# Kernel tuning notes

Hardware: AMD Instinct MI355X
Metric: run time of the kernel (lower is better)

The kernel has to match this reference:

```python
import jax, jax.numpy as jnp
import numpy as np

GAMMA = 0.96875      # retention decay, 1 - 2**-5
GROUPS = 8           # config.group_norm_num
EPS = 1e-6           # config.retention_group_norm_eps


def _get_D(T, dtype):
    # D[n, m] = gamma**(n-m) for n >= m else 0 (causal exponential decay)
    n = jnp.arange(T)[:, None]
    m = jnp.arange(T)[None, :]
    log_g = jnp.log(jnp.asarray(GAMMA, dtype))
    # where-select avoids inf*0 NaNs for n < m (matches D[D != D] = 0)
    return jnp.where(n >= m, jnp.exp((n - m).astype(dtype) * log_g),
                     jnp.zeros((), dtype))


def _group_norm(x, w, b):
    # x: (N, C); torch.nn.GroupNorm semantics (biased variance, affine)
    N, C = x.shape
    xg = x.reshape(N, GROUPS, C // GROUPS)
    mu = xg.mean(-1, keepdims=True)
    var = xg.var(-1, keepdims=True)
    xn = ((xg - mu) * jax.lax.rsqrt(var + EPS)).reshape(N, C)
    return xn * w + b


def setup_inputs() -> dict:
    key = jax.random.key(0)
    k0, k1, k2, k3, k4 = jax.random.split(key, 5)
    B, T, C = 2, 8192, 64
    Q_in = jax.random.normal(k0, (B, T, C), jnp.float32)
    W_Q = jax.random.normal(k1, (C, C), jnp.float32) / C
    W_K = jax.random.normal(k2, (C, C), jnp.float32) / C
    W_V = jax.random.normal(k3, (C, C), jnp.float32) / C
    gn_weight = 1.0 + 0.02 * jax.random.normal(k4, (C,), jnp.float32)
    gn_bias = jnp.zeros((C,), jnp.float32)
    return {"Q_in": Q_in, "W_Q": W_Q, "W_K": W_K, "W_V": W_V,
            "gn_weight": gn_weight, "gn_bias": gn_bias}


def reference(Q_in, W_Q, W_K, W_V, gn_weight, gn_bias):
    B, T, C = Q_in.shape
    # _qkv with KV_in=None, act='none'
    Q = Q_in @ W_Q
    K = Q_in @ W_K
    V = Q_in @ W_V
    # retention scores with multiplicative causal decay mask
    QK = jnp.einsum("btc,bsc->bts", Q, K) * _get_D(T, Q.dtype)[None]
    out = jnp.einsum("bts,bsc->btc", QK, V)  # (B, T, C)
    # _out: dropout(p=0) -> GroupNorm over flattened (B*T, C) -> transpose+view
    out = _group_norm(out.reshape(-1, C), gn_weight, gn_bias).reshape(B, T, C)
    out = jnp.swapaxes(out, -2, -1).reshape(B, T, C)  # faithful to .transpose().view()
    return out
```

## Files before the change

### kernel.cpp

```cpp
#include <hip/hip_runtime.h>


constexpr int SEQ = 8192;
constexpr int CH  = 64;
constexpr float LOG2G = -0.045803690f;

typedef __attribute__((ext_vector_type(8))) _Float16     half8;
typedef __attribute__((ext_vector_type(4))) float        f32x4;
typedef __attribute__((ext_vector_type(4))) unsigned int u32x4;

__device__ inline unsigned short f2h(float x) {
    _Float16 h = (_Float16)x;
    return __builtin_bit_cast(unsigned short, h);
}

__global__ __launch_bounds__(256) void qkv_kernel(
    const float* __restrict__ Xin, const float* __restrict__ Wq,
    const float* __restrict__ Wk, const float* __restrict__ Wv,
    unsigned short* __restrict__ Qh, unsigned short* __restrict__ Kh,
    unsigned short* __restrict__ Vt)
{
    __shared__ unsigned short sWt[3][64][72];
    const int tid = threadIdx.x;
    const size_t row0 = (size_t)blockIdx.x * 64;
    const int b  = (int)(row0 >> 13);
    const int t0 = (int)(row0 & (SEQ - 1));

    {
        const int c  = tid & 63;
        const int k0 = (tid >> 6) * 2;
        #pragma unroll
        for (int m = 0; m < 3; ++m) {
            const float* W = (m == 0) ? Wq : ((m == 1) ? Wk : Wv);
            #pragma unroll
            for (int it = 0; it < 8; ++it) {
                const int k = k0 + it * 8;
                const unsigned lo = f2h(W[k * 64 + c]);
                const unsigned hi = f2h(W[(k + 1) * 64 + c]);
                *(unsigned int*)&sWt[m][c][k] = lo | (hi << 16);
            }
        }
    }

    const int l15 = tid & 15, q4 = (tid >> 4) & 3, wvi = tid >> 6;

    half8 xf[2];
    {
        const float* Xp = Xin + (row0 + (size_t)(wvi * 16 + l15)) * 64;
        #pragma unroll
        for (int h = 0; h < 2; ++h) {
            const f32x4 a  = *(const f32x4*)(Xp + h * 32 + q4 * 8);
            const f32x4 bb = *(const f32x4*)(Xp + h * 32 + q4 * 8 + 4);
            half8 t;
            t[0] = (_Float16)a[0];  t[1] = (_Float16)a[1];
            t[2] = (_Float16)a[2];  t[3] = (_Float16)a[3];
            t[4] = (_Float16)bb[0]; t[5] = (_Float16)bb[1];
            t[6] = (_Float16)bb[2]; t[7] = (_Float16)bb[3];
            xf[h] = t;
        }
    }
    __syncthreads();

    const int trow = (int)row0 + wvi * 16;
    #pragma unroll
    for (int m = 0; m < 2; ++m) {
        unsigned short* O = (m == 0) ? Qh : Kh;
        #pragma unroll
        for (int ct = 0; ct < 4; ++ct) {
            const half8 wf0 = *(const half8*)&sWt[m][ct * 16 + l15][q4 * 8];
            const half8 wf1 = *(const half8*)&sWt[m][ct * 16 + l15][32 + q4 * 8];
            f32x4 d = {0.f, 0.f, 0.f, 0.f};
            d = __builtin_amdgcn_mfma_f32_16x16x32_f16(xf[0], wf0, d, 0, 0, 0);
            d = __builtin_amdgcn_mfma_f32_16x16x32_f16(xf[1], wf1, d, 0, 0, 0);
            #pragma unroll
            for (int i = 0; i < 4; ++i)
                O[(size_t)(trow + q4 * 4 + i) * 64 + ct * 16 + l15] = f2h(d[i]);
        }
    }
    #pragma unroll
    for (int mt = 0; mt < 4; ++mt) {
        const half8 wf0 = *(const half8*)&sWt[2][mt * 16 + l15][q4 * 8];
        const half8 wf1 = *(const half8*)&sWt[2][mt * 16 + l15][32 + q4 * 8];
        f32x4 d = {0.f, 0.f, 0.f, 0.f};
        d = __builtin_amdgcn_mfma_f32_16x16x32_f16(wf0, xf[0], d, 0, 0, 0);
        d = __builtin_amdgcn_mfma_f32_16x16x32_f16(wf1, xf[1], d, 0, 0, 0);
        #pragma unroll
        for (int i = 0; i < 4; ++i)
            Vt[(size_t)(b * 64 + mt * 16 + q4 * 4 + i) * SEQ + t0 + wvi * 16 + l15] = f2h(d[i]);
    }
}

__global__ __launch_bounds__(256, 4) void attn_kernel(
    const unsigned short* __restrict__ Qh, const unsigned short* __restrict__ Kh,
    const unsigned short* __restrict__ Vt,
    const float* __restrict__ gnw, const float* __restrict__ gnb,
    float* __restrict__ out)
{
    __shared__ unsigned int sS[4][16][44];
    __shared__ float sO[4][16][68];
    __shared__ float sGW[64], sGB[64];

    const int tid  = threadIdx.x;
    const int w    = tid >> 6;
    const int lane = tid & 63;
    const int l15  = lane & 15, q4 = lane >> 4;
    const int tile = blockIdx.x;
    const int b    = tile >> 9;
    const int t0   = (tile & 511) << 4;

    if (tid < 64) { sGW[tid] = gnw[tid]; sGB[tid] = gnb[tid]; }

    const unsigned short* Qp = Qh + (size_t)(b * SEQ + t0 + l15) * 64 + q4 * 8;
    const half8 qf0 = *(const half8*)Qp;
    const half8 qf1 = *(const half8*)(Qp + 32);

    float g0[4];
    #pragma unroll
    for (int i = 0; i < 4; ++i)
        g0[i] = exp2f((float)(l15 - q4 * 4 - i) * LOG2G);
    const float c16 = exp2f(-16.f * LOG2G);
    const float c32 = c16 * c16;
    const float c48 = c32 * c16;

    f32x4 acc[4];
    #pragma unroll
    for (int ct = 0; ct < 4; ++ct) acc[ct] = (f32x4){0.f, 0.f, 0.f, 0.f};

    const int cs_hi = t0 >> 6;
    const int cs_lo = (cs_hi >= 16) ? cs_hi - 16 : 0;
    const unsigned short* Kbase = Kh + (size_t)b * SEQ * 64;
    const unsigned short* Vbase = Vt + (size_t)b * 64 * SEQ;

    for (int cs = cs_lo + w; cs <= cs_hi; cs += 4) {
        const int s0 = cs << 6;

        half8 kf[4][2];
        #pragma unroll
        for (int st = 0; st < 4; ++st) {
            const unsigned short* p = Kbase + (size_t)(s0 + st * 16 + l15) * 64 + q4 * 8;
            kf[st][0] = *(const half8*)p;
            kf[st][1] = *(const half8*)(p + 32);
        }
        f32x4 sv[4];
        #pragma unroll
        for (int st = 0; st < 4; ++st) {
            f32x4 s = {0.f, 0.f, 0.f, 0.f};
            s = __builtin_amdgcn_mfma_f32_16x16x32_f16(kf[st][0], qf0, s, 0, 0, 0);
            s = __builtin_amdgcn_mfma_f32_16x16x32_f16(kf[st][1], qf1, s, 0, 0, 0);
            sv[st] = s;
        }

        half8 vf[4][2];
        #pragma unroll
        for (int ct = 0; ct < 4; ++ct) {
            const unsigned short* p = Vbase + (size_t)(ct * 16 + l15) * SEQ + s0 + q4 * 8;
            vf[ct][0] = *(const half8*)p;
            vf[ct][1] = *(const half8*)(p + 32);
        }

        const float gbase = exp2f((float)(t0 - s0) * LOG2G);
        const float gs[4] = {gbase, gbase * c16, gbase * c32, gbase * c48};
        if (cs < cs_hi) {
            #pragma unroll
            for (int st = 0; st < 4; ++st) {
                const unsigned u0 = (unsigned)f2h(sv[st][0] * (gs[st] * g0[0]))
                                  | ((unsigned)f2h(sv[st][1] * (gs[st] * g0[1])) << 16);
                const unsigned u1 = (unsigned)f2h(sv[st][2] * (gs[st] * g0[2]))
                                  | ((unsigned)f2h(sv[st][3] * (gs[st] * g0[3])) << 16);
                sS[w][l15][st * 8 + q4 * 2]     = u0;
                sS[w][l15][st * 8 + q4 * 2 + 1] = u1;
            }
        } else {
            const int dbase = t0 + l15 - s0;
            #pragma unroll
            for (int st = 0; st < 4; ++st) {
                float wt[4];
                #pragma unroll
                for (int i = 0; i < 4; ++i) {
                    const int srel = st * 16 + q4 * 4 + i;
                    wt[i] = (dbase - srel >= 0) ? gs[st] * g0[i] : 0.f;
                }
                const unsigned u0 = (unsigned)f2h(sv[st][0] * wt[0])
                                  | ((unsigned)f2h(sv[st][1] * wt[1]) << 16);
                const unsigned u1 = (unsigned)f2h(sv[st][2] * wt[2])
                                  | ((unsigned)f2h(sv[st][3] * wt[3]) << 16);
                sS[w][l15][st * 8 + q4 * 2]     = u0;
                sS[w][l15][st * 8 + q4 * 2 + 1] = u1;
            }
        }

        asm volatile("s_waitcnt lgkmcnt(0)" ::: "memory");

        const u32x4 ua0 = *(const u32x4*)&sS[w][l15][q4 * 4];
        const u32x4 ua1 = *(const u32x4*)&sS[w][l15][16 + q4 * 4];
        const half8 af0 = __builtin_bit_cast(half8, ua0);
        const half8 af1 = __builtin_bit_cast(half8, ua1);
        #pragma unroll
        for (int ct = 0; ct < 4; ++ct) {
            acc[ct] = __builtin_amdgcn_mfma_f32_16x16x32_f16(af0, vf[ct][0], acc[ct], 0, 0, 0);
            acc[ct] = __builtin_amdgcn_mfma_f32_16x16x32_f16(af1, vf[ct][1], acc[ct], 0, 0, 0);
        }
    }

    #pragma unroll
    for (int ct = 0; ct < 4; ++ct) {
        #pragma unroll
        for (int i = 0; i < 4; ++i)
            sO[w][q4 * 4 + i][ct * 16 + l15] = acc[ct][i];
    }
    __syncthreads();
    {
        const int r = tid >> 4, c4 = (tid & 15) * 4;
        f32x4 v = *(const f32x4*)&sO[0][r][c4];
        v += *(const f32x4*)&sO[1][r][c4];
        v += *(const f32x4*)&sO[2][r][c4];
        v += *(const f32x4*)&sO[3][r][c4];
        *(f32x4*)&sO[0][r][c4] = v;
    }
    __syncthreads();
    if (tid < 128) {
        const int r = tid >> 3, g = tid & 7;
        float x[8];
        float s = 0.f, ss = 0.f;
        #pragma unroll
        for (int j = 0; j < 8; ++j) {
            x[j] = sO[0][r][g * 8 + j];
            s += x[j]; ss += x[j] * x[j];
        }
        const float mu  = s * 0.125f;
        const float var = ss * 0.125f - mu * mu;
        const float rs  = rsqrtf(var + 1e-6f);
        #pragma unroll
        for (int j = 0; j < 8; ++j) {
            const int c = g * 8 + j;
            sO[0][r][c] = (x[j] - mu) * rs * sGW[c] + sGB[c];
        }
    }
    __syncthreads();
    #pragma unroll
    for (int pass = 0; pass < 4; ++pass) {
        const int c = pass * 16 + (tid >> 4);
        const int t = tid & 15;
        out[(size_t)(b * 64 + c) * SEQ + t0 + t] = sO[0][t][c];
    }
}

extern "C" void kernel_launch(void* const* d_in, const int* in_sizes, int n_in,
                              void* d_out, int out_size, void* d_ws, size_t ws_size,
                              hipStream_t stream)
{
    const float* Xin = (const float*)d_in[0];
    const float* Wq  = (const float*)d_in[1];
    const float* Wk  = (const float*)d_in[2];
    const float* Wv  = (const float*)d_in[3];
    const float* gnw = (const float*)d_in[4];
    const float* gnb = (const float*)d_in[5];

    const size_t NROW = (size_t)2 * SEQ;
    unsigned short* Qh = (unsigned short*)d_ws;
    unsigned short* Kh = Qh + NROW * CH;
    unsigned short* Vt = Kh + NROW * CH;

    qkv_kernel<<<dim3(256), dim3(256), 0, stream>>>(Xin, Wq, Wk, Wv, Qh, Kh, Vt);
    attn_kernel<<<dim3(1024), dim3(256), 0, stream>>>(Qh, Kh, Vt, gnw, gnb, (float*)d_out);
}
```

Before: 102.8 us.

## Split QKV projection across per-matrix waves with register-held weights

Restructures the QKV projection kernel so each block handles 16 rows with three waves, one each for Q, K and V. Each wave loads and converts its weight matrix straight into registers, which removes the shared-memory staging and the block barrier. The grid grows from 256 to 1024 blocks for more parallelism. In exchange, weight loads from global memory are repeated per block and are strided (uncoalesced), though they should mostly hit in cache.

```diff
diff --git a/kernel.cpp b/kernel.cpp
--- a/kernel.cpp
+++ b/kernel.cpp
@@ -14,79 +14,73 @@
     return __builtin_bit_cast(unsigned short, h);
 }
 
-__global__ __launch_bounds__(256) void qkv_kernel(
+__global__ __launch_bounds__(192) void qkv_kernel(
     const float* __restrict__ Xin, const float* __restrict__ Wq,
     const float* __restrict__ Wk, const float* __restrict__ Wv,
     unsigned short* __restrict__ Qh, unsigned short* __restrict__ Kh,
     unsigned short* __restrict__ Vt)
 {
-    __shared__ unsigned short sWt[3][64][72];
-    const int tid = threadIdx.x;
-    const size_t row0 = (size_t)blockIdx.x * 64;
+    const int tid  = threadIdx.x;
+    const int role = tid >> 6;
+    const int lane = tid & 63;
+    const int l15  = lane & 15, q4 = lane >> 4;
+    const size_t row0 = (size_t)blockIdx.x * 16;
     const int b  = (int)(row0 >> 13);
     const int t0 = (int)(row0 & (SEQ - 1));
 
-    {
-        const int c  = tid & 63;
-        const int k0 = (tid >> 6) * 2;
-        #pragma unroll
-        for (int m = 0; m < 3; ++m) {
-            const float* W = (m == 0) ? Wq : ((m == 1) ? Wk : Wv);
-            #pragma unroll
-            for (int it = 0; it < 8; ++it) {
-                const int k = k0 + it * 8;
-                const unsigned lo = f2h(W[k * 64 + c]);
-                const unsigned hi = f2h(W[(k + 1) * 64 + c]);
-                *(unsigned int*)&sWt[m][c][k] = lo | (hi << 16);
-            }
-        }
-    }
-
-    const int l15 = tid & 15, q4 = (tid >> 4) & 3, wvi = tid >> 6;
-
     half8 xf[2];
     {
-        const float* Xp = Xin + (row0 + (size_t)(wvi * 16 + l15)) * 64;
+        const float* Xp = Xin + (row0 + l15) * 64;
         #pragma unroll
         for (int h = 0; h < 2; ++h) {
-            const f32x4 a  = *(const f32x4*)(Xp + h * 32 + q4 * 8);
-            const f32x4 bb = *(const f32x4*)(Xp + h * 32 + q4 * 8 + 4);
+            const f32x4 a = *(const f32x4*)(Xp + h * 32 + q4 * 8);
+            const f32x4 c = *(const f32x4*)(Xp + h * 32 + q4 * 8 + 4);
             half8 t;
-            t[0] = (_Float16)a[0];  t[1] = (_Float16)a[1];
-            t[2] = (_Float16)a[2];  t[3] = (_Float16)a[3];
-            t[4] = (_Float16)bb[0]; t[5] = (_Float16)bb[1];
-            t[6] = (_Float16)bb[2]; t[7] = (_Float16)bb[3];
+            t[0] = (_Float16)a[0]; t[1] = (_Float16)a[1];
+            t[2] = (_Float16)a[2]; t[3] = (_Float16)a[3];
+            t[4] = (_Float16)c[0]; t[5] = (_Float16)c[1];
+            t[6] = (_Float16)c[2]; t[7] = (_Float16)c[3];
             xf[h] = t;
         }
     }
-    __syncthreads();
-
-    const int trow = (int)row0 + wvi * 16;
-    #pragma unroll
-    for (int m = 0; m < 2; ++m) {
-        unsigned short* O = (m == 0) ? Qh : Kh;
+
+    const float* W = (role == 0) ? Wq : ((role == 1) ? Wk : Wv);
+    half8 wf[4][2];
+    #pragma unroll
+    for (int ct = 0; ct < 4; ++ct) {
+        const int c = ct * 16 + l15;
+        #pragma unroll
+        for (int kh = 0; kh < 2; ++kh) {
+            const int k0 = kh * 32 + q4 * 8;
+            half8 t;
+            #pragma unroll
+            for (int j = 0; j < 8; ++j)
+                t[j] = (_Float16)W[(k0 + j) * 64 + c];
+            wf[ct][kh] = t;
+        }
+    }
+
+    if (role < 2) {
+        unsigned short* O = (role == 0) ? Qh : Kh;
         #pragma unroll
         for (int ct = 0; ct < 4; ++ct) {
-            const half8 wf0 = *(const half8*)&sWt[m][ct * 16 + l15][q4 * 8];
-            const half8 wf1 = *(const half8*)&sWt[m][ct * 16 + l15][32 + q4 * 8];
             f32x4 d = {0.f, 0.f, 0.f, 0.f};
-            d = __builtin_amdgcn_mfma_f32_16x16x32_f16(xf[0], wf0, d, 0, 0, 0);
-            d = __builtin_amdgcn_mfma_f32_16x16x32_f16(xf[1], wf1, d, 0, 0, 0);
+            d = __builtin_amdgcn_mfma_f32_16x16x32_f16(xf[0], wf[ct][0], d, 0, 0, 0);
+            d = __builtin_amdgcn_mfma_f32_16x16x32_f16(xf[1], wf[ct][1], d, 0, 0, 0);
             #pragma unroll
             for (int i = 0; i < 4; ++i)
-                O[(size_t)(trow + q4 * 4 + i) * 64 + ct * 16 + l15] = f2h(d[i]);
-        }
-    }
-    #pragma unroll
-    for (int mt = 0; mt < 4; ++mt) {
-        const half8 wf0 = *(const half8*)&sWt[2][mt * 16 + l15][q4 * 8];
-        const half8 wf1 = *(const half8*)&sWt[2][mt * 16 + l15][32 + q4 * 8];
-        f32x4 d = {0.f, 0.f, 0.f, 0.f};
-        d = __builtin_amdgcn_mfma_f32_16x16x32_f16(wf0, xf[0], d, 0, 0, 0);
-        d = __builtin_amdgcn_mfma_f32_16x16x32_f16(wf1, xf[1], d, 0, 0, 0);
-        #pragma unroll
-        for (int i = 0; i < 4; ++i)
-            Vt[(size_t)(b * 64 + mt * 16 + q4 * 4 + i) * SEQ + t0 + wvi * 16 + l15] = f2h(d[i]);
+                O[(row0 + q4 * 4 + i) * 64 + ct * 16 + l15] = f2h(d[i]);
+        }
+    } else {
+        #pragma unroll
+        for (int mt = 0; mt < 4; ++mt) {
+            f32x4 d = {0.f, 0.f, 0.f, 0.f};
+            d = __builtin_amdgcn_mfma_f32_16x16x32_f16(wf[mt][0], xf[0], d, 0, 0, 0);
+            d = __builtin_amdgcn_mfma_f32_16x16x32_f16(wf[mt][1], xf[1], d, 0, 0, 0);
+            #pragma unroll
+            for (int i = 0; i < 4; ++i)
+                Vt[(size_t)(b * 64 + mt * 16 + q4 * 4 + i) * SEQ + t0 + l15] = f2h(d[i]);
+        }
     }
 }
 
@@ -261,6 +255,6 @@
     unsigned short* Kh = Qh + NROW * CH;
     unsigned short* Vt = Kh + NROW * CH;
 
-    qkv_kernel<<<dim3(256), dim3(256), 0, stream>>>(Xin, Wq, Wk, Wv, Qh, Kh, Vt);
+    qkv_kernel<<<dim3(1024), dim3(192), 0, stream>>>(Xin, Wq, Wk, Wv, Qh, Kh, Vt);
     attn_kernel<<<dim3(1024), dim3(256), 0, stream>>>(Qh, Kh, Vt, gnw, gnb, (float*)d_out);
 }
```

Result: no change. 103.7 us (+0.8%).
